# Kernel tuning notes

Measured on AMD Instinct MI355X. Metric: run time of the kernel, lower is better.

## Reference

```python
import jax, jax.numpy as jnp
import numpy as np

B, S, D, H = 8, 1024, 1024, 16
HD = D // H  # head_dim = 64


def setup_inputs() -> dict:
    key = jax.random.key(0)
    ks = jax.random.split(key, 5)
    scale = 1.0 / np.sqrt(D)
    return {
        "x": jax.random.normal(ks[0], (B, S, D), dtype=jnp.float32),
        "wq": jax.random.normal(ks[1], (D, D), dtype=jnp.float32) * scale,
        "wk": jax.random.normal(ks[2], (D, D), dtype=jnp.float32) * scale,
        "wv": jax.random.normal(ks[3], (D, D), dtype=jnp.float32) * scale,
        "wo": jax.random.normal(ks[4], (D, D), dtype=jnp.float32) * scale,
    }


def reference(x, wq, wk, wv, wo):
    b, s, d = x.shape
    # nn.Linear: y = x @ W.T  (weights stored [out, in])
    q = (x @ wq.T).reshape(b, s, H, HD).transpose(0, 2, 1, 3)  # [b,h,s,hd]
    k = (x @ wk.T).reshape(b, s, H, HD).transpose(0, 2, 1, 3)
    v = (x @ wv.T).reshape(b, s, H, HD).transpose(0, 2, 1, 3)
    scores = jnp.einsum("bhqd,bhkd->bhqk", q, k) / jnp.sqrt(jnp.float32(HD))
    attn = jax.nn.softmax(scores, axis=-1)  # dropout p=0.0 -> identity
    out = jnp.einsum("bhqk,bhkd->bhqd", attn, v)
    out = out.transpose(0, 2, 1, 3).reshape(b, s, d)
    return out @ wo.T
```

## Files before the change

kernel.cpp:

```cpp
#include <hip/hip_runtime.h>
#include <hip/hip_bf16.h>
#include <math.h>

#define BB 8
#define SS 1024
#define DD 1024
#define HH 16
#define HDIM 64
#define MM (BB * SS)
#define QSCALE 0.1803368801111204f

typedef __attribute__((ext_vector_type(8))) short s8v;
typedef __attribute__((ext_vector_type(4))) short s4v;
typedef __attribute__((ext_vector_type(4))) float f4v;

#define GLD16(g, l)                                                            \
  __builtin_amdgcn_global_load_lds(                                            \
      (const __attribute__((address_space(1))) void*)(g),                      \
      (__attribute__((address_space(3))) void*)(l), 16, 0, 0)

__device__ __forceinline__ unsigned short bf16_ru(float f) {
  return (unsigned short)((__float_as_uint(f) + 0x8000u) >> 16);
}

__device__ __forceinline__ unsigned bf16_pack2(float f0, float f1) {
#if __has_builtin(__builtin_amdgcn_perm)
  unsigned a = __float_as_uint(f0) + 0x8000u;
  unsigned b = __float_as_uint(f1) + 0x8000u;
  return __builtin_amdgcn_perm(b, a, 0x07060302u);
#else
  return (unsigned)bf16_ru(f0) | ((unsigned)bf16_ru(f1) << 16);
#endif
}

__device__ __forceinline__ float fast_exp2(float x) {
  return __builtin_amdgcn_exp2f(x);
}

__global__ void cast_all(const float* __restrict__ x, const float* __restrict__ wq,
                         const float* __restrict__ wk, const float* __restrict__ wv,
                         const float* __restrict__ wo, __hip_bfloat16* __restrict__ xb,
                         __hip_bfloat16* __restrict__ wqkvb,
                         __hip_bfloat16* __restrict__ wob) {
  int blk = blockIdx.x;
  const float* src;
  __hip_bfloat16* dst;
  int base;
  if (blk < 2048) {
    src = x; dst = xb; base = blk * 4096;
  } else if (blk < 2304) {
    src = wq; dst = wqkvb; base = (blk - 2048) * 4096;
  } else if (blk < 2560) {
    src = wk; dst = wqkvb + (1 << 20); base = (blk - 2304) * 4096;
  } else if (blk < 2816) {
    src = wv; dst = wqkvb + (2 << 20); base = (blk - 2560) * 4096;
  } else {
    src = wo; dst = wob; base = (blk - 2816) * 4096;
  }
#pragma unroll
  for (int it = 0; it < 4; ++it) {
    int idx = base + it * 1024 + threadIdx.x * 4;
    float4 f = *(const float4*)&src[idx];
    *(uint2*)&dst[idx] = uint2{bf16_pack2(f.x, f.y), bf16_pack2(f.z, f.w)};
  }
}

template <int MODE>
__global__ __launch_bounds__(256, (MODE == 0 ? 4 : 3)) void gemm_bt(
    const __hip_bfloat16* __restrict__ A, const __hip_bfloat16* __restrict__ Bm,
    float* __restrict__ Cf, __hip_bfloat16* __restrict__ Qo,
    __hip_bfloat16* __restrict__ Ko, __hip_bfloat16* __restrict__ Vt) {
  __shared__ __hip_bfloat16 smem[2][128 * 64];
  __hip_bfloat16* sA = smem[0];
  __hip_bfloat16* sB = smem[1];

  const int tid = threadIdx.x;
  const int wave = tid >> 6;
  const int lane = tid & 63;
  const int l15 = lane & 15;
  const int quad = lane >> 4;
  const int c8 = lane & 7;
  const int r8 = lane >> 3;

  constexpr int GX = (MODE == 0) ? 16 : 8;
  constexpr int NWG = GX * 64;
  const int id = blockIdx.y * GX + blockIdx.x;
  const int nid = (id & 7) * (NWG / 8) + (id >> 3);
  const int m0 = (nid / GX) * 128;
  const int n0 = (nid % GX) * 128;

  const int wm = (wave >> 1) * 64;
  const int wn = (wave & 1) * 64;

  f4v acc[4][4];
#pragma unroll
  for (int i = 0; i < 4; ++i)
#pragma unroll
    for (int j = 0; j < 4; ++j) acc[i][j] = {0.f, 0.f, 0.f, 0.f};

  for (int kt = 0; kt < DD / 64; ++kt) {
    const int k0 = kt * 64;
    __syncthreads();
#pragma unroll
    for (int r = 0; r < 4; ++r) {
      int rb = r * 32 + wave * 8;
      int row = rb + r8;
      int scol = (c8 ^ (row & 7)) * 8;
      GLD16(A + (size_t)(m0 + row) * DD + k0 + scol, &sA[rb * 64]);
      GLD16(Bm + (size_t)(n0 + row) * DD + k0 + scol, &sB[rb * 64]);
    }
    __syncthreads();

#pragma unroll
    for (int kk = 0; kk < 2; ++kk) {
      s8v af[4], bf[4];
#pragma unroll
      for (int i = 0; i < 4; ++i)
        af[i] = *(const s8v*)&sA[(wm + i * 16 + l15) * 64 +
                                 (((kk * 4 + quad) ^ (l15 & 7)) * 8)];
#pragma unroll
      for (int j = 0; j < 4; ++j)
        bf[j] = *(const s8v*)&sB[(wn + j * 16 + l15) * 64 +
                                 (((kk * 4 + quad) ^ (l15 & 7)) * 8)];
#pragma unroll
      for (int i = 0; i < 4; ++i)
#pragma unroll
        for (int j = 0; j < 4; ++j)
          acc[i][j] = (MODE == 2)
                          ? __builtin_amdgcn_mfma_f32_16x16x32_bf16(af[i], bf[j],
                                                                    acc[i][j], 0, 0, 0)
                          : __builtin_amdgcn_mfma_f32_16x16x32_bf16(bf[j], af[i],
                                                                    acc[i][j], 0, 0, 0);
    }
  }

  if constexpr (MODE == 1) {
#pragma unroll
    for (int i = 0; i < 4; ++i) {
#pragma unroll
      for (int j = 0; j < 4; ++j) {
        const int s_abs = m0 + wm + i * 16 + l15;
        const int col = n0 + wn + j * 16 + quad * 4;
        float4 f4 = {acc[i][j][0], acc[i][j][1], acc[i][j][2], acc[i][j][3]};
        *(float4*)&Cf[(size_t)s_abs * DD + col] = f4;
      }
    }
  } else {
    __syncthreads();
    char* epc = (char*)smem + wave * 8192;
    const float scl = (MODE == 0) ? ((n0 < 1024) ? QSCALE : 1.0f) : 1.0f;
#pragma unroll
    for (int i = 0; i < 4; ++i) {
#pragma unroll
      for (int j = 0; j < 4; ++j) {
        const int r = (MODE == 0 ? i : j) * 16 + l15;
        const int c0 = (MODE == 0 ? j : i) * 16 + quad * 4;
        const int off = r * 128 + (((c0 >> 3) ^ (r & 7)) << 4) + ((c0 & 7) * 2);
        *(uint2*)(epc + off) =
            uint2{bf16_pack2(acc[i][j][0] * scl, acc[i][j][1] * scl),
                  bf16_pack2(acc[i][j][2] * scl, acc[i][j][3] * scl)};
      }
    }
    asm volatile("s_waitcnt lgkmcnt(0)" ::: "memory");
    const int rr8 = lane >> 3;
    const int ch = (lane & 7) ^ rr8;
    const int h = ((n0 + wn) & 1023) >> 6;
    const int sb = m0 + wm;
    const int b = sb >> 10, s0 = sb & 1023;
    if constexpr (MODE == 0) {
      const bool isQ = (n0 < 1024);
      __hip_bfloat16* dst =
          (isQ ? Qo : Ko) + ((size_t)(b * HH + h) * SS + s0) * HDIM;
#pragma unroll
      for (int it = 0; it < 8; ++it) {
        const int r = it * 8 + rr8;
        uint4 vv = *(const uint4*)(epc + r * 128 + ch * 16);
        *(uint4*)&dst[(size_t)r * HDIM + (lane & 7) * 8] = vv;
      }
    } else {
      __hip_bfloat16* dst = Vt + (size_t)(b * HH + h) * HDIM * SS + s0;
#pragma unroll
      for (int it = 0; it < 8; ++it) {
        const int r = it * 8 + rr8;
        uint4 vv = *(const uint4*)(epc + r * 128 + ch * 16);
        *(uint4*)&dst[(size_t)r * SS + (lane & 7) * 8] = vv;
      }
    }
  }
}

#define KPLD 76
__global__ __launch_bounds__(256, 4) void attn_kernel(
    const __hip_bfloat16* __restrict__ Q, const __hip_bfloat16* __restrict__ K,
    const __hip_bfloat16* __restrict__ Vt, __hip_bfloat16* __restrict__ Oout) {
  __shared__ __hip_bfloat16 sK[64 * 64];
  __shared__ __hip_bfloat16 sVt[64 * 64];
  __shared__ unsigned short sP[4 * 32 * KPLD];

  const int tid = threadIdx.x;
  const int wave = tid >> 6;
  const int lane = tid & 63;
  const int l15 = lane & 15;
  const int quad = lane >> 4;
  const int c8 = lane & 7;
  const int r8 = lane >> 3;

  const int bh = blockIdx.x;
  const int q0 = blockIdx.y * 128;
  const size_t head = (size_t)bh * SS * HDIM;

  unsigned short* sPw = &sP[wave * 32 * KPLD];

  s8v qf[2][2];
#pragma unroll
  for (int mf = 0; mf < 2; ++mf) {
    int s = q0 + wave * 32 + mf * 16 + l15;
#pragma unroll
    for (int kk = 0; kk < 2; ++kk)
      qf[mf][kk] = *(const s8v*)&Q[head + (size_t)s * HDIM + kk * 32 + quad * 8];
  }

  s8v onesB;
#pragma unroll
  for (int j = 0; j < 8; ++j) onesB[j] = (short)0x3F80;

  f4v o[2][4];
  f4v lacc[2];
#pragma unroll
  for (int mf = 0; mf < 2; ++mf) {
    lacc[mf] = {0.f, 0.f, 0.f, 0.f};
#pragma unroll
    for (int f = 0; f < 4; ++f) o[mf][f] = {0.f, 0.f, 0.f, 0.f};
  }

  for (int kb = 0; kb < SS / 64; ++kb) {
    __syncthreads();
#pragma unroll
    for (int r = 0; r < 2; ++r) {
      int rb = r * 32 + wave * 8;
      int row = rb + r8;
      int sc8 = (c8 ^ (row & 7)) * 8;
      GLD16(&K[head + (size_t)(kb * 64 + row) * HDIM + sc8], &sK[rb * 64]);
      GLD16(&Vt[head + (size_t)row * SS + kb * 64 + sc8], &sVt[rb * 64]);
    }
    __syncthreads();

    f4v sc[2][4];
#pragma unroll
    for (int mf = 0; mf < 2; ++mf)
#pragma unroll
      for (int f = 0; f < 4; ++f) sc[mf][f] = {0.f, 0.f, 0.f, 0.f};
#pragma unroll
    for (int kk = 0; kk < 2; ++kk) {
#pragma unroll
      for (int f = 0; f < 4; ++f) {
        s8v kf = *(const s8v*)&sK[(f * 16 + l15) * 64 +
                                  (((kk * 4 + quad) ^ (l15 & 7)) * 8)];
#pragma unroll
        for (int mf = 0; mf < 2; ++mf)
          sc[mf][f] =
              __builtin_amdgcn_mfma_f32_16x16x32_bf16(kf, qf[mf][kk], sc[mf][f], 0, 0, 0);
      }
    }

#pragma unroll
    for (int mf = 0; mf < 2; ++mf)
#pragma unroll
      for (int f = 0; f < 4; ++f) {
        float p0 = fast_exp2(sc[mf][f][0]), p1 = fast_exp2(sc[mf][f][1]);
        float p2 = fast_exp2(sc[mf][f][2]), p3 = fast_exp2(sc[mf][f][3]);
        *(uint2*)&sPw[(mf * 16 + l15) * KPLD + f * 16 + quad * 4] =
            uint2{bf16_pack2(p0, p1), bf16_pack2(p2, p3)};
      }

#pragma unroll
    for (int kk = 0; kk < 2; ++kk) {
      s8v pf[2];
#pragma unroll
      for (int mf = 0; mf < 2; ++mf) {
        const unsigned short* p = &sPw[(mf * 16 + l15) * KPLD + kk * 32 + quad * 8];
        s4v lo = *(const s4v*)p;
        s4v hi = *(const s4v*)(p + 4);
        pf[mf] = __builtin_shufflevector(lo, hi, 0, 1, 2, 3, 4, 5, 6, 7);
        lacc[mf] = __builtin_amdgcn_mfma_f32_16x16x32_bf16(pf[mf], onesB, lacc[mf], 0, 0, 0);
      }
#pragma unroll
      for (int f = 0; f < 4; ++f) {
        s8v vf = *(const s8v*)&sVt[(f * 16 + l15) * 64 +
                                   (((kk * 4 + quad) ^ (l15 & 7)) * 8)];
#pragma unroll
        for (int mf = 0; mf < 2; ++mf)
          o[mf][f] =
              __builtin_amdgcn_mfma_f32_16x16x32_bf16(pf[mf], vf, o[mf][f], 0, 0, 0);
      }
    }
  }

  const int b = bh >> 4, h = bh & 15;
  char* epw = (char*)sPw;
#pragma unroll
  for (int mf = 0; mf < 2; ++mf) {
    float rl[4];
#pragma unroll
    for (int r = 0; r < 4; ++r) rl[r] = 1.0f / lacc[mf][r];
#pragma unroll
    for (int f = 0; f < 4; ++f)
#pragma unroll
      for (int r = 0; r < 4; ++r) {
        const int row = mf * 16 + quad * 4 + r;
        const int off =
            row * 128 + (((2 * f + (l15 >> 3)) ^ (row & 7)) << 4) + ((l15 & 7) * 2);
        *(unsigned short*)(epw + off) = bf16_ru(o[mf][f][r] * rl[r]);
      }
  }
  asm volatile("s_waitcnt lgkmcnt(0)" ::: "memory");
  const int rr8 = lane >> 3;
  unsigned short* dstO = (unsigned short*)Oout +
                         (size_t)(b * SS + q0 + wave * 32) * DD + h * HDIM;
#pragma unroll
  for (int it = 0; it < 4; ++it) {
    const int row = it * 8 + rr8;
    uint4 vv = *(const uint4*)(epw + row * 128 + (((lane & 7) ^ rr8) << 4));
    *(uint4*)&dstO[(size_t)row * DD + (lane & 7) * 8] = vv;
  }
}

extern "C" void kernel_launch(void* const* d_in, const int* in_sizes, int n_in,
                              void* d_out, int out_size, void* d_ws, size_t ws_size,
                              hipStream_t stream) {
  const float* x = (const float*)d_in[0];
  const float* wq = (const float*)d_in[1];
  const float* wk = (const float*)d_in[2];
  const float* wv = (const float*)d_in[3];
  const float* wo = (const float*)d_in[4];

  char* ws = (char*)d_ws;
  __hip_bfloat16* xb = (__hip_bfloat16*)(ws);
  __hip_bfloat16* wqkvb = (__hip_bfloat16*)(ws + (16 << 20));
  __hip_bfloat16* wob = (__hip_bfloat16*)(ws + (22 << 20));
  __hip_bfloat16* qh = (__hip_bfloat16*)(ws + (24 << 20));
  __hip_bfloat16* kh = (__hip_bfloat16*)(ws + (40 << 20));
  __hip_bfloat16* vt = (__hip_bfloat16*)(ws + (56 << 20));
  __hip_bfloat16* attnO = (__hip_bfloat16*)(ws + (72 << 20));

  cast_all<<<3072, 256, 0, stream>>>(x, wq, wk, wv, wo, xb, wqkvb, wob);

  gemm_bt<0><<<dim3(16, 64), 256, 0, stream>>>(xb, wqkvb, nullptr, qh, kh, nullptr);
  gemm_bt<2><<<dim3(8, 64), 256, 0, stream>>>(xb, wqkvb + (2 << 20), nullptr,
                                              nullptr, nullptr, vt);

  attn_kernel<<<dim3(BB * HH, SS / 128), 256, 0, stream>>>(qh, kh, vt, attnO);

  gemm_bt<1><<<dim3(8, 64), 256, 0, stream>>>(attnO, wob, (float*)d_out, nullptr,
                                              nullptr, nullptr);
}
```

Baseline: 219.2 us.

## Add 256x256-tile 8-wave Q/K projection GEMM with interleaved double-buffered loads

Replaces the 128x128 Q/K projection GEMM with a dedicated kernel using 256x256 output tiles, 512 threads (8 waves each computing 128x64), and a 128KB LDS double buffer. Global-to-LDS loads for the next k-tile are split into quarter chunks interleaved between MFMA phases with explicit vmcnt waits, raw barriers and setprio. This aims to raise arithmetic intensity and overlap memory with compute. The costs are lower occupancy (1-2 blocks per CU given the LDS use) and only 256 blocks, which may underfill the CUs.

```diff
diff --git a/kernel.cpp b/kernel.cpp
--- a/kernel.cpp
+++ b/kernel.cpp
@@ -18,6 +18,13 @@
   __builtin_amdgcn_global_load_lds(                                            \
       (const __attribute__((address_space(1))) void*)(g),                      \
       (__attribute__((address_space(3))) void*)(l), 16, 0, 0)
+
+#define BARRIER()                                                              \
+  do {                                                                         \
+    asm volatile("" ::: "memory");                                             \
+    __builtin_amdgcn_s_barrier();                                              \
+    asm volatile("" ::: "memory");                                             \
+  } while (0)
 
 __device__ __forceinline__ unsigned short bf16_ru(float f) {
   return (unsigned short)((__float_as_uint(f) + 0x8000u) >> 16);
@@ -65,14 +72,10 @@
   }
 }
 
-template <int MODE>
-__global__ __launch_bounds__(256, (MODE == 0 ? 4 : 3)) void gemm_bt(
+__global__ __launch_bounds__(512, 2) void gemm_qk8(
     const __hip_bfloat16* __restrict__ A, const __hip_bfloat16* __restrict__ Bm,
-    float* __restrict__ Cf, __hip_bfloat16* __restrict__ Qo,
-    __hip_bfloat16* __restrict__ Ko, __hip_bfloat16* __restrict__ Vt) {
-  __shared__ __hip_bfloat16 smem[2][128 * 64];
-  __hip_bfloat16* sA = smem[0];
-  __hip_bfloat16* sB = smem[1];
+    __hip_bfloat16* __restrict__ Qo, __hip_bfloat16* __restrict__ Ko) {
+  __shared__ char smem[131072];
 
   const int tid = threadIdx.x;
   const int wave = tid >> 6;
@@ -82,7 +85,169 @@
   const int c8 = lane & 7;
   const int r8 = lane >> 3;
 
-  constexpr int GX = (MODE == 0) ? 16 : 8;
+  const int id = blockIdx.y * 8 + blockIdx.x;
+  const int nid = (id & 7) * 32 + (id >> 3);
+  const int m0 = (nid >> 3) * 256;
+  const int n0 = (nid & 7) * 256;
+
+  const int wm = (wave >> 2) * 128;
+  const int wn = (wave & 3) * 64;
+
+  auto stA = [&](int t, int r) {
+    const int row = r * 64 + wave * 8 + r8;
+    const int sc = (c8 ^ (row & 7)) * 8;
+    GLD16(A + (size_t)(m0 + row) * DD + t * 64 + sc,
+          smem + (t & 1) * 65536 + (r * 64 + wave * 8) * 128);
+  };
+  auto stB = [&](int t, int r) {
+    const int row = r * 64 + wave * 8 + r8;
+    const int sc = (c8 ^ (row & 7)) * 8;
+    GLD16(Bm + (size_t)(n0 + row) * DD + t * 64 + sc,
+          smem + (t & 1) * 65536 + 32768 + (r * 64 + wave * 8) * 128);
+  };
+
+  f4v acc[8][4];
+#pragma unroll
+  for (int i = 0; i < 8; ++i)
+#pragma unroll
+    for (int j = 0; j < 4; ++j) acc[i][j] = {0.f, 0.f, 0.f, 0.f};
+
+  stB(0, 0); stB(0, 1);
+  stB(0, 2); stB(0, 3);
+  stA(0, 0); stA(0, 2);
+  stA(0, 1); stA(0, 3);
+  stB(1, 0); stB(1, 1);
+  stB(1, 2); stB(1, 3);
+  asm volatile("s_waitcnt vmcnt(6)" ::: "memory");
+  BARRIER();
+
+  for (int t = 0; t < 16; ++t) {
+    char* bufA = smem + (t & 1) * 65536;
+    char* bufB = bufA + 32768;
+    s8v bfr[2][4];
+    s8v af[4];
+
+#pragma unroll
+    for (int kk = 0; kk < 2; ++kk)
+#pragma unroll
+      for (int j = 0; j < 4; ++j)
+        bfr[kk][j] = *(const s8v*)(bufB + (size_t)(wn + j * 16 + l15) * 128 +
+                                   (((kk * 4 + quad) ^ (l15 & 7)) << 4));
+#pragma unroll
+    for (int mi = 0; mi < 4; ++mi)
+      af[mi] = *(const s8v*)(bufA + (size_t)(wm + mi * 16 + l15) * 128 +
+                             ((quad ^ (l15 & 7)) << 4));
+    if (t < 15) { stA(t + 1, 0); stA(t + 1, 2); }
+    BARRIER();
+    __builtin_amdgcn_s_setprio(1);
+#pragma unroll
+    for (int mi = 0; mi < 4; ++mi)
+#pragma unroll
+      for (int j = 0; j < 4; ++j)
+        acc[mi][j] = __builtin_amdgcn_mfma_f32_16x16x32_bf16(bfr[0][j], af[mi],
+                                                             acc[mi][j], 0, 0, 0);
+    __builtin_amdgcn_s_setprio(0);
+    if (t == 15) asm volatile("s_waitcnt vmcnt(0)" ::: "memory");
+    else         asm volatile("s_waitcnt vmcnt(6)" ::: "memory");
+    BARRIER();
+
+#pragma unroll
+    for (int mi = 0; mi < 4; ++mi)
+      af[mi] = *(const s8v*)(bufA + (size_t)(wm + 64 + mi * 16 + l15) * 128 +
+                             ((quad ^ (l15 & 7)) << 4));
+    if (t < 15) { stA(t + 1, 1); stA(t + 1, 3); }
+    BARRIER();
+    __builtin_amdgcn_s_setprio(1);
+#pragma unroll
+    for (int mi = 0; mi < 4; ++mi)
+#pragma unroll
+      for (int j = 0; j < 4; ++j)
+        acc[4 + mi][j] = __builtin_amdgcn_mfma_f32_16x16x32_bf16(
+            bfr[0][j], af[mi], acc[4 + mi][j], 0, 0, 0);
+    __builtin_amdgcn_s_setprio(0);
+    BARRIER();
+
+#pragma unroll
+    for (int mi = 0; mi < 4; ++mi)
+      af[mi] = *(const s8v*)(bufA + (size_t)(wm + mi * 16 + l15) * 128 +
+                             (((4 + quad) ^ (l15 & 7)) << 4));
+    if (t < 14) { stB(t + 2, 0); stB(t + 2, 1); }
+    BARRIER();
+    __builtin_amdgcn_s_setprio(1);
+#pragma unroll
+    for (int mi = 0; mi < 4; ++mi)
+#pragma unroll
+      for (int j = 0; j < 4; ++j)
+        acc[mi][j] = __builtin_amdgcn_mfma_f32_16x16x32_bf16(bfr[1][j], af[mi],
+                                                             acc[mi][j], 0, 0, 0);
+    __builtin_amdgcn_s_setprio(0);
+    BARRIER();
+
+#pragma unroll
+    for (int mi = 0; mi < 4; ++mi)
+      af[mi] = *(const s8v*)(bufA + (size_t)(wm + 64 + mi * 16 + l15) * 128 +
+                             (((4 + quad) ^ (l15 & 7)) << 4));
+    if (t < 14) { stB(t + 2, 2); stB(t + 2, 3); }
+    BARRIER();
+    __builtin_amdgcn_s_setprio(1);
+#pragma unroll
+    for (int mi = 0; mi < 4; ++mi)
+#pragma unroll
+      for (int j = 0; j < 4; ++j)
+        acc[4 + mi][j] = __builtin_amdgcn_mfma_f32_16x16x32_bf16(
+            bfr[1][j], af[mi], acc[4 + mi][j], 0, 0, 0);
+    __builtin_amdgcn_s_setprio(0);
+    if (t < 14)       asm volatile("s_waitcnt vmcnt(6)" ::: "memory");
+    else if (t == 14) asm volatile("s_waitcnt vmcnt(2)" ::: "memory");
+    BARRIER();
+  }
+
+  const bool isQ = (n0 < 1024);
+  const float scl = isQ ? QSCALE : 1.0f;
+  const int h = ((n0 + wn) & 1023) >> 6;
+  const int sb = m0 + wm;
+  const int b = sb >> 10, s0 = sb & 1023;
+  char* epc = smem + wave * 16384;
+#pragma unroll
+  for (int i = 0; i < 8; ++i) {
+#pragma unroll
+    for (int j = 0; j < 4; ++j) {
+      const int r = i * 16 + l15;
+      const int c0 = j * 16 + quad * 4;
+      const int off = r * 128 + (((c0 >> 3) ^ (r & 7)) << 4) + ((c0 & 7) * 2);
+      *(uint2*)(epc + off) =
+          uint2{bf16_pack2(acc[i][j][0] * scl, acc[i][j][1] * scl),
+                bf16_pack2(acc[i][j][2] * scl, acc[i][j][3] * scl)};
+    }
+  }
+  asm volatile("s_waitcnt lgkmcnt(0)" ::: "memory");
+  __hip_bfloat16* dst = (isQ ? Qo : Ko) + ((size_t)(b * HH + h) * SS + s0) * HDIM;
+#pragma unroll
+  for (int it = 0; it < 16; ++it) {
+    const int r = it * 8 + r8;
+    uint4 vv = *(const uint4*)(epc + r * 128 + (((lane & 7) ^ r8) << 4));
+    *(uint4*)&dst[(size_t)r * HDIM + (lane & 7) * 8] = vv;
+  }
+}
+
+template <int MODE>
+__global__ __launch_bounds__(256, 3) void gemm_bt(
+    const __hip_bfloat16* __restrict__ A, const __hip_bfloat16* __restrict__ Bm,
+    float* __restrict__ Cf, __hip_bfloat16* __restrict__ Qo,
+    __hip_bfloat16* __restrict__ Ko, __hip_bfloat16* __restrict__ Vt) {
+  __shared__ __hip_bfloat16 smem[2][128 * 64];
+  __hip_bfloat16* sA = smem[0];
+  __hip_bfloat16* sB = smem[1];
+
+  const int tid = threadIdx.x;
+  const int wave = tid >> 6;
+  const int lane = tid & 63;
+  const int l15 = lane & 15;
+  const int quad = lane >> 4;
+  const int c8 = lane & 7;
+  const int r8 = lane >> 3;
+
+  constexpr int GX = 8;
   constexpr int NWG = GX * 64;
   const int id = blockIdx.y * GX + blockIdx.x;
   const int nid = (id & 7) * (NWG / 8) + (id >> 3);
@@ -148,17 +313,15 @@
   } else {
     __syncthreads();
     char* epc = (char*)smem + wave * 8192;
-    const float scl = (MODE == 0) ? ((n0 < 1024) ? QSCALE : 1.0f) : 1.0f;
 #pragma unroll
     for (int i = 0; i < 4; ++i) {
 #pragma unroll
       for (int j = 0; j < 4; ++j) {
-        const int r = (MODE == 0 ? i : j) * 16 + l15;
-        const int c0 = (MODE == 0 ? j : i) * 16 + quad * 4;
+        const int r = j * 16 + l15;
+        const int c0 = i * 16 + quad * 4;
         const int off = r * 128 + (((c0 >> 3) ^ (r & 7)) << 4) + ((c0 & 7) * 2);
-        *(uint2*)(epc + off) =
-            uint2{bf16_pack2(acc[i][j][0] * scl, acc[i][j][1] * scl),
-                  bf16_pack2(acc[i][j][2] * scl, acc[i][j][3] * scl)};
+        *(uint2*)(epc + off) = uint2{bf16_pack2(acc[i][j][0], acc[i][j][1]),
+                                     bf16_pack2(acc[i][j][2], acc[i][j][3])};
       }
     }
     asm volatile("s_waitcnt lgkmcnt(0)" ::: "memory");
@@ -167,24 +330,12 @@
     const int h = ((n0 + wn) & 1023) >> 6;
     const int sb = m0 + wm;
     const int b = sb >> 10, s0 = sb & 1023;
-    if constexpr (MODE == 0) {
-      const bool isQ = (n0 < 1024);
-      __hip_bfloat16* dst =
-          (isQ ? Qo : Ko) + ((size_t)(b * HH + h) * SS + s0) * HDIM;
-#pragma unroll
-      for (int it = 0; it < 8; ++it) {
-        const int r = it * 8 + rr8;
-        uint4 vv = *(const uint4*)(epc + r * 128 + ch * 16);
-        *(uint4*)&dst[(size_t)r * HDIM + (lane & 7) * 8] = vv;
-      }
-    } else {
-      __hip_bfloat16* dst = Vt + (size_t)(b * HH + h) * HDIM * SS + s0;
-#pragma unroll
-      for (int it = 0; it < 8; ++it) {
-        const int r = it * 8 + rr8;
-        uint4 vv = *(const uint4*)(epc + r * 128 + ch * 16);
-        *(uint4*)&dst[(size_t)r * SS + (lane & 7) * 8] = vv;
-      }
+    __hip_bfloat16* dst = Vt + (size_t)(b * HH + h) * HDIM * SS + s0;
+#pragma unroll
+    for (int it = 0; it < 8; ++it) {
+      const int r = it * 8 + rr8;
+      uint4 vv = *(const uint4*)(epc + r * 128 + ch * 16);
+      *(uint4*)&dst[(size_t)r * SS + (lane & 7) * 8] = vv;
     }
   }
 }
@@ -345,7 +496,7 @@
 
   cast_all<<<3072, 256, 0, stream>>>(x, wq, wk, wv, wo, xb, wqkvb, wob);
 
-  gemm_bt<0><<<dim3(16, 64), 256, 0, stream>>>(xb, wqkvb, nullptr, qh, kh, nullptr);
+  gemm_qk8<<<dim3(8, 32), 512, 0, stream>>>(xb, wqkvb, qh, kh);
   gemm_bt<2><<<dim3(8, 64), 256, 0, stream>>>(xb, wqkvb + (2 << 20), nullptr,
                                               nullptr, nullptr, vt);
 
```

After: 211.9 us. -3.4%, faster.
